# Kernel tuning notes

Measured on AMD Instinct MI355X. Metric: run time of the kernel, lower is better.

Reference implementation:

```python
import jax, jax.numpy as jnp
import numpy as np

B, R, C, D = 8, 64, 16, 128  # batch, num_rows(taxa), patch_num, embed_dim


def _linear_init(key, fan_in, fan_out):
    lim = 1.0 / np.sqrt(fan_in)
    kw, kb = jax.random.split(key)
    W = jax.random.uniform(kw, (fan_in, fan_out), jnp.float32, -lim, lim)
    b = jax.random.uniform(kb, (fan_out,), jnp.float32, -lim, lim)
    return W, b


def setup_inputs() -> dict:
    key = jax.random.key(0)
    ks = jax.random.split(key, 8)
    row_np, col_np = np.triu_indices(R, k=1)  # n = R*(R-1)/2 = 2016 pairs
    hW, hb = _linear_init(ks[1], D, D)
    gW, gb = _linear_init(ks[2], D, D)
    qW, qb = _linear_init(ks[3], D, D)
    kW, kb = _linear_init(ks[4], D, D)
    s1W, s1b = _linear_init(ks[5], D, D)
    s2W, s2b = _linear_init(ks[6], D, 1)
    return {
        "batch_input": jax.random.normal(ks[0], (B, R, C, D), jnp.float32),
        "seq_mask": jnp.ones((B, 1, C), jnp.float32),
        "row": jnp.asarray(row_np, jnp.int32),
        "col": jnp.asarray(col_np, jnp.int32),
        "hW": hW, "hb": hb, "gW": gW, "gb": gb,
        "qW": qW, "qb": qb, "kW": kW, "kb": kb,
        "s1W": s1W, "s1b": s1b, "s2W": s2W, "s2b": s2b,
    }


def reference(batch_input, seq_mask, row, col,
              hW, hb, gW, gb, qW, qb, kW, kb, s1W, s1b, s2W, s2b):
    b, r, c, d = batch_input.shape
    n = row.shape[0]
    # pairwise gather: x_i, x_j -> [b, n, c, d]
    x_i = batch_input[:, row]
    x_j = batch_input[:, col]
    # sigmoid gate fusion of the pair
    h = (x_i - x_j) @ hW + hb
    z = jax.nn.sigmoid(h)
    x = z * x_i + (1.0 - z) * x_j
    # masked global attention over the batch_input 'memory' (r > 2 branch)
    q = x @ qW + qb                    # [b, n, c, d]
    k = batch_input @ kW + kb          # [b, r, c, d]
    scale = 1.0 / np.sqrt(d * c).astype(np.float32)
    alpha = jnp.einsum('bncd,brcd->bnr', q, k) * scale
    # -inf at (pair n, rows row[n] and col[n]); equivalent to += -inf on finite scores
    neg_mask = (jnp.zeros((n, r), bool)
                .at[jnp.arange(n), row].set(True)
                .at[jnp.arange(n), col].set(True))
    alpha = jnp.where(neg_mask[None], -jnp.inf, alpha)
    alpha = jax.nn.softmax(alpha, axis=-1)
    x_glob = jnp.einsum('bnr,brcd->bncd', alpha, batch_input)
    g = x_glob @ gW + gb
    w = jax.nn.sigmoid(g)
    x = (1.0 - w) * x + w * x_glob
    # s_out: Linear -> GELU(exact) -> Linear(d,1), then mask and reduce over c
    s = jax.nn.gelu(x @ s1W + s1b, approximate=False) @ s2W + s2b  # [b, n, c, 1]
    scores = s[..., 0] * seq_mask       # seq_mask [b,1,c] broadcasts over n
    return scores.sum(-1)               # [b, n]
```

## Files before the change

kernel.cpp:

```cpp
#include <hip/hip_runtime.h>
#include <hip/hip_bf16.h>
#include <math.h>

#define B_    8
#define R_    64
#define C_    16
#define D_    128
#define NPAIR 2016
#define CD    2048
#define PG    32
#define NPG   63
#define XSTR  136
#define LSTR  68
#define NEG_BIG (-1e30f)
#define SCALE 0.022097086912079608f

typedef __attribute__((ext_vector_type(8))) short short8;
typedef __attribute__((ext_vector_type(4))) float float4v;

#define WMH  0u
#define WML  16384u
#define WSH  98304u
#define VECO 131072u
#define QBKO 131592u
#define MO   132616u
#define XTO  1181192u
#define GTO  2229768u
#define HO   3278344u

__device__ __forceinline__ unsigned short f2b(float f){
    union { float f; unsigned int u; } v; v.f = f;
    const unsigned int r = v.u + 0x7FFFu + ((v.u >> 16) & 1u);
    return (unsigned short)(r >> 16);
}
__device__ __forceinline__ float b2f(unsigned short u){
    union { unsigned int i; float f; } v; v.i = ((unsigned int)u) << 16; return v.f;
}
__device__ __forceinline__ float lo2f(unsigned int u){
    union { unsigned int i; float f; } v; v.i = u << 16; return v.f;
}
__device__ __forceinline__ float hif2f(unsigned int u){
    union { unsigned int i; float f; } v; v.i = u & 0xffff0000u; return v.f;
}
__device__ __forceinline__ unsigned int pack2(float a, float b){
    unsigned int r;
    asm("v_cvt_pk_bf16_f32 %0, %1, %2" : "=v"(r) : "v"(a), "v"(b));
    return r;
}
__device__ __forceinline__ unsigned short f2b1(float a){
    unsigned int r;
    asm("v_cvt_pk_bf16_f32 %0, %1, %1" : "=v"(r) : "v"(a));
    return (unsigned short)r;
}
__device__ __forceinline__ void split_bf(float v, float* hi, float* lo){
    union { float f; unsigned int u; } x; x.f = v;
    const unsigned int r = (x.u + 0x7FFFu + ((x.u >> 16) & 1u)) & 0xffff0000u;
    union { unsigned int u; float f; } h; h.u = r;
    *hi = h.f; *lo = v - h.f;
}
__device__ __forceinline__ void splitw(float v, short* h, short* l){
    union { float f; unsigned int u; } x; x.f = v;
    const unsigned int rh = (x.u + 0x7FFFu + ((x.u >> 16) & 1u)) & 0xffff0000u;
    union { unsigned int u; float f; } hf; hf.u = rh;
    *h = (short)(rh >> 16);
    *l = (short)f2b(v - hf.f);
}
__device__ __forceinline__ float sigmoid_safe(float x){
    return __builtin_amdgcn_rcpf(1.f + __expf(-x));
}
__device__ __forceinline__ float gelu_tanh(float x){
    const float u = x*x;
    const float g2 = x*(1.5957691216057308f + 0.07135481627159f*u);
    return x * sigmoid_safe(g2);
}

__global__ __launch_bounds__(256) void k_prepA(
    const float* __restrict__ qW, const float* __restrict__ qb,
    const float* __restrict__ kW, const float* __restrict__ kb,
    unsigned short* __restrict__ ws)
{
    const int bid = blockIdx.x, t = threadIdx.x;
    if (bid < 64){
        __shared__ float sKW[2][128];
        const int e0 = bid*2;
        sKW[t>>7][t&127] = kW[(e0 + (t>>7))*128 + (t&127)];
        __syncthreads();
        const int e = t>>7, d = t&127;
        const float* qr = qW + d*128;
        const float* kr = sKW[e];
        float acc = 0.f;
        #pragma unroll 8
        for (int g = 0; g < 128; g += 4){
            const float4 qv = *reinterpret_cast<const float4*>(qr + g);
            acc += qv.x*kr[g] + qv.y*kr[g+1] + qv.z*kr[g+2] + qv.w*kr[g+3];
        }
        float hi, lo; split_bf(acc, &hi, &lo);
        ws[WMH + d*128 + (e0+e)] = f2b(hi);
        ws[WML + d*128 + (e0+e)] = f2b(lo);
    } else {
        float* vec = (float*)(ws + VECO);
        if (t < 128){
            float a1 = 0.f, a2 = 0.f;
            #pragma unroll 8
            for (int g = 0; g < 128; g += 4){
                const float4 q4 = *reinterpret_cast<const float4*>(qW + t*128 + g);
                const float4 k4 = *reinterpret_cast<const float4*>(kW + t*128 + g);
                const float4 kb4 = *reinterpret_cast<const float4*>(kb + g);
                const float4 qb4 = *reinterpret_cast<const float4*>(qb + g);
                a1 += q4.x*kb4.x + q4.y*kb4.y + q4.z*kb4.z + q4.w*kb4.w;
                a2 += k4.x*qb4.x + k4.y*qb4.y + k4.z*qb4.z + k4.w*qb4.w;
            }
            vec[t] = a1;
            vec[128 + t] = a2;
        } else if (t == 128){
            float a = 0.f;
            for (int g = 0; g < 128; ++g) a = fmaf(qb[g], kb[g], a);
            vec[256] = a;
        }
    }
}

__global__ __launch_bounds__(512) void k_prepB(const float* __restrict__ x,
        const float* __restrict__ hW, const float* __restrict__ gW,
        const float* __restrict__ gb, const float* __restrict__ s1W,
        unsigned short* __restrict__ ws)
{
    __shared__ __align__(16) unsigned short smem[8832];
    __shared__ float sQ[4];
    const int bid = blockIdx.x, t = threadIdx.x;
    const int w = t >> 6, lane = t & 63, l15 = lane & 15, quad = lane >> 4;

    if (bid < 128){
        unsigned short* sH = smem;
        const int br0 = bid * 4;
        const float* kqf = (const float*)(ws + VECO) + 128;
        const float* mbf = (const float*)(ws + VECO);
        if (t < 4) sQ[t] = 0.f;
        __syncthreads();
        float qacc[4] = {0.f, 0.f, 0.f, 0.f};
        #pragma unroll
        for (int i = 0; i < 4; ++i){
            const int flat = (t + 512*i)*4;
            const int lr = i;
            const int cd = flat & 2047;
            const float4 v = *reinterpret_cast<const float4*>(x + (size_t)(br0+lr)*CD + cd);
            const int ad = (lr*16 + (cd>>7))*XSTR + lr*8 + (cd & 127);
            uint2 uh;
            uh.x = pack2(v.x, v.y); uh.y = pack2(v.z, v.w);
            *reinterpret_cast<uint2*>(sH + ad) = uh;
            const float4 kq4 = *reinterpret_cast<const float4*>(kqf + (cd & 127));
            qacc[i] = v.x*kq4.x + v.y*kq4.y + v.z*kq4.z + v.w*kq4.w;
        }
        #pragma unroll
        for (int i = 0; i < 4; ++i){
            float s = qacc[i];
            #pragma unroll
            for (int off = 1; off < 64; off <<= 1) s += __shfl_xor(s, off);
            if (lane == 0) atomicAdd(&sQ[i], s);
        }
        __syncthreads();
        {
            const float bv = mbf[w*16 + l15];
            float4v acc[4];
            #pragma unroll
            for (int mt = 0; mt < 4; ++mt){ float4v d = {bv,bv,bv,bv}; acc[mt] = d; }
            #pragma unroll
            for (int ks = 0; ks < 4; ++ks){
                const int ko = ks*32 + quad*8;
                const int bd = (w*16 + l15)*128 + ko;
                const short8 bh = *reinterpret_cast<const short8*>(ws + WMH + bd);
                const short8 bl = *reinterpret_cast<const short8*>(ws + WML + bd);
                #pragma unroll
                for (int mt = 0; mt < 4; ++mt){
                    const int ad = (mt*16 + l15)*XSTR + mt*8 + ko;
                    const short8 ah = *reinterpret_cast<const short8*>(sH + ad);
                    float4v d = acc[mt];
                    d = __builtin_amdgcn_mfma_f32_16x16x32_bf16(ah, bh, d, 0,0,0);
                    d = __builtin_amdgcn_mfma_f32_16x16x32_bf16(ah, bl, d, 0,0,0);
                    acc[mt] = d;
                }
            }
            const int f = w*16 + l15;
            #pragma unroll
            for (int mt = 0; mt < 4; ++mt)
            #pragma unroll
            for (int e = 0; e < 4; ++e){
                const int c = quad*4 + e;
                ws[MO + (size_t)(br0+mt)*CD + c*128 + f] = f2b(acc[mt][e]);
            }
            if (t < 4){
                const float s0 = ((const float*)(ws + VECO))[256];
                ((float*)(ws + QBKO))[br0 + t] = sQ[t] + 16.f*s0;
            }
        }
        {
            const int n = w*16 + l15;
            float4v acc[4];
            #pragma unroll
            for (int mt = 0; mt < 4; ++mt){ float4v z = {0.f,0.f,0.f,0.f}; acc[mt] = z; }
            #pragma unroll
            for (int ks = 0; ks < 4; ++ks){
                const int ko = ks*32 + quad*8;
                short8 bh, bl;
                #pragma unroll
                for (int j = 0; j < 8; ++j){
                    short hh, ll;
                    splitw(hW[(size_t)(ko+j)*128 + n], &hh, &ll);
                    bh[j] = hh; bl[j] = ll;
                }
                #pragma unroll
                for (int mt = 0; mt < 4; ++mt){
                    const int ad = (mt*16 + l15)*XSTR + mt*8 + ko;
                    const short8 ah = *reinterpret_cast<const short8*>(sH + ad);
                    float4v d = acc[mt];
                    d = __builtin_amdgcn_mfma_f32_16x16x32_bf16(ah, bh, d, 0,0,0);
                    d = __builtin_amdgcn_mfma_f32_16x16x32_bf16(ah, bl, d, 0,0,0);
                    acc[mt] = d;
                }
            }
            #pragma unroll
            for (int mt = 0; mt < 4; ++mt)
            #pragma unroll
            for (int e = 0; e < 4; ++e){
                const int c = quad*4 + e;
                ws[HO + (size_t)(br0+mt)*CD + c*128 + n] = f2b(acc[mt][e]);
            }
        }
    } else if (bid < 256){
        unsigned short* tileB = smem;
        const int gidx = bid - 128;
        const int b = gidx >> 4, cd0 = (gidx & 15)*128;
        #pragma unroll
        for (int i = 0; i < 16; ++i){
            const int idx = i*512 + t;
            const int r = idx >> 7, dd = idx & 127;
            tileB[r*138 + dd] = f2b(x[(size_t)(b*64 + r)*CD + cd0 + dd]);
        }
        __syncthreads();
        {
            const unsigned int base = XTO + (unsigned int)(b*2048 + cd0)*64;
            #pragma unroll
            for (int j = 0; j < 16; ++j){
                const int idx = j*512 + t;
                const int cc = idx >> 6, r = idx & 63;
                ws[base + cc*64 + r] = tileB[r*138 + cc];
            }
        }
        const int fA = w*16 + l15;
        float4v acc[4];
        #pragma unroll
        for (int nt = 0; nt < 4; ++nt){ float4v z = {0.f,0.f,0.f,0.f}; acc[nt] = z; }
        #pragma unroll
        for (int ks = 0; ks < 4; ++ks){
            const int ko = ks*32 + quad*8;
            short8 ah, al;
            #pragma unroll
            for (int j = 0; j < 8; ++j){
                short hh, ll;
                splitw(gW[(size_t)(ko+j)*128 + fA], &hh, &ll);
                ah[j] = hh; al[j] = ll;
            }
            #pragma unroll
            for (int nt = 0; nt < 4; ++nt){
                const short8 bb = *reinterpret_cast<const short8*>(tileB + (nt*16 + l15)*138 + ko);
                float4v d = acc[nt];
                d = __builtin_amdgcn_mfma_f32_16x16x32_bf16(ah, bb, d, 0,0,0);
                d = __builtin_amdgcn_mfma_f32_16x16x32_bf16(al, bb, d, 0,0,0);
                acc[nt] = d;
            }
        }
        #pragma unroll
        for (int nt = 0; nt < 4; ++nt)
        #pragma unroll
        for (int e = 0; e < 4; ++e){
            const int f = w*16 + quad*4 + e;
            const float val = acc[nt][e] + gb[f];
            ws[GTO + (size_t)(b*2048 + cd0 + f)*64 + nt*16 + l15] = f2b(val);
        }
    } else {
        const int gid = (bid - 256)*4096 + t;
        #pragma unroll
        for (int i = 0; i < 8; ++i){
            const int g = gid + i*512;
            const int n = g >> 7, k = g & 127;
            ws[WSH + g] = f2b(s1W[k*128 + n]);
        }
    }
}

__global__ __launch_bounds__(1024, 4) void k_main(
    const float* __restrict__ x, const float* __restrict__ seq_mask,
    const int* __restrict__ row, const int* __restrict__ col,
    const float* __restrict__ hb, const float* __restrict__ s1b,
    const float* __restrict__ s2W, const float* __restrict__ s2b,
    const unsigned short* __restrict__ ws, float* __restrict__ out)
{
    __shared__ __align__(16) unsigned short sX[512*XSTR + 256];
    __shared__ __align__(16) unsigned short sAl[32*72];
    __shared__ float sLog[32*LSTR];
    __shared__ float sOut[PG];
    __shared__ float sMask[16];
    __shared__ int srp[PG], scp[PG];

    const int t = threadIdx.x;
    const int w = t >> 6, lane = t & 63, l15 = lane & 15, quad = lane >> 4;
    const int b = blockIdx.x, p0 = blockIdx.y * PG;
    const float* xb = x + (size_t)b * R_ * CD;
    const unsigned short* Hb = ws + HO + (size_t)b * R_ * CD;

    if (t < PG){ srp[t] = row[p0+t]; scp[t] = col[p0+t]; sOut[t] = 0.f; }
    if (t >= 32 && t < 48) sMask[t-32] = seq_mask[b*C_ + (t-32)];
    for (int i = t; i < 32*72; i += 1024) sAl[i] = 0;
    for (int i = t; i < 32*LSTR; i += 1024) sLog[i] = 0.f;
    __syncthreads();

    #pragma unroll 4
    for (int i = 0; i < 16; ++i){
        const int flat = (t + 1024*i)*4;
        const int p = flat >> 11, cd = flat & 2047;
        const int ri = srp[p], ci = scp[p];
        const float4 xi = *reinterpret_cast<const float4*>(xb + (size_t)ri*CD + cd);
        const float4 xj = *reinterpret_cast<const float4*>(xb + (size_t)ci*CD + cd);
        const uint2 Hi2 = *reinterpret_cast<const uint2*>(Hb + (size_t)ri*CD + cd);
        const uint2 Hj2 = *reinterpret_cast<const uint2*>(Hb + (size_t)ci*CD + cd);
        const float4 h4 = *reinterpret_cast<const float4*>(hb + (cd & 127));
        const float z0 = sigmoid_safe(lo2f(Hi2.x)  - lo2f(Hj2.x)  + h4.x);
        const float z1 = sigmoid_safe(hif2f(Hi2.x) - hif2f(Hj2.x) + h4.y);
        const float z2 = sigmoid_safe(lo2f(Hi2.y)  - lo2f(Hj2.y)  + h4.z);
        const float z3 = sigmoid_safe(hif2f(Hi2.y) - hif2f(Hj2.y) + h4.w);
        const float v0 = xj.x + z0*(xi.x - xj.x);
        const float v1 = xj.y + z1*(xi.y - xj.y);
        const float v2 = xj.z + z2*(xi.z - xj.z);
        const float v3 = xj.w + z3*(xi.w - xj.w);
        const int ad = (p*16 + (cd>>7))*XSTR + p*8 + (cd & 127);
        uint2 uv; uv.x = pack2(v0,v1); uv.y = pack2(v2,v3);
        *reinterpret_cast<uint2*>(sX + ad) = uv;
    }
    __syncthreads();

    {
        const int rt = w & 3, kh = w >> 2;
        const int r = rt*16 + l15;
        const unsigned short* Mr = ws + MO + ((size_t)b*64 + r)*CD + kh*512;
        float4v d0a = {0.f,0.f,0.f,0.f}, d0b = {0.f,0.f,0.f,0.f};
        float4v d1a = {0.f,0.f,0.f,0.f}, d1b = {0.f,0.f,0.f,0.f};
        #pragma unroll
        for (int h = 0; h < 2; ++h){
            short8 bhr[8];
            #pragma unroll
            for (int u = 0; u < 8; ++u)
                bhr[u] = *reinterpret_cast<const short8*>(Mr + (h*8+u)*32 + quad*8);
            #pragma unroll
            for (int u = 0; u < 8; ++u){
                const int k = kh*512 + (h*8+u)*32 + quad*8;
                const int khi = k >> 7, klo = k & 127;
                const int pA = l15, pB = 16 + l15;
                const short8 ahA = *reinterpret_cast<const short8*>(
                    sX + (pA*16 + khi)*XSTR + pA*8 + klo);
                const short8 ahB = *reinterpret_cast<const short8*>(
                    sX + (pB*16 + khi)*XSTR + pB*8 + klo);
                if (u & 1){
                    d0b = __builtin_amdgcn_mfma_f32_16x16x32_bf16(ahA, bhr[u], d0b, 0,0,0);
                    d1b = __builtin_amdgcn_mfma_f32_16x16x32_bf16(ahB, bhr[u], d1b, 0,0,0);
                } else {
                    d0a = __builtin_amdgcn_mfma_f32_16x16x32_bf16(ahA, bhr[u], d0a, 0,0,0);
                    d1a = __builtin_amdgcn_mfma_f32_16x16x32_bf16(ahB, bhr[u], d1a, 0,0,0);
                }
            }
        }
        const float4v dA = d0a + d0b;
        const float4v dB = d1a + d1b;
        #pragma unroll
        for (int e = 0; e < 4; ++e){
            const int pp = quad*4 + e;
            atomicAdd(&sLog[pp*LSTR + r], dA[e]);
            atomicAdd(&sLog[(16+pp)*LSTR + r], dB[e]);
        }
    }
    __syncthreads();

    const unsigned short* XTb = ws + XTO + (size_t)b * CD * 64;
    const unsigned short* GTb = ws + GTO + (size_t)b * CD * 64;
    short8 px0[2], px1[2], pg0[2], pg1[2];
    #pragma unroll
    for (int j = 0; j < 2; ++j){
        const int cd = w*128 + j*16 + l15;
        px0[j] = *reinterpret_cast<const short8*>(XTb + (size_t)cd*64 + quad*8);
        px1[j] = *reinterpret_cast<const short8*>(XTb + (size_t)cd*64 + 32 + quad*8);
        pg0[j] = *reinterpret_cast<const short8*>(GTb + (size_t)cd*64 + quad*8);
        pg1[j] = *reinterpret_cast<const short8*>(GTb + (size_t)cd*64 + 32 + quad*8);
    }

    if (t < 512){
        const int pp = t >> 4, l = t & 15;
        const int ri = srp[pp], ci = scp[pp];
        const float* qbk = (const float*)(ws + QBKO);
        float v[4]; float m = NEG_BIG;
        #pragma unroll
        for (int k = 0; k < 4; ++k){
            const int r = l + 16*k;
            float lv = (sLog[pp*LSTR + r] + qbk[b*64 + r]) * SCALE;
            if (r == ri || r == ci) lv = NEG_BIG;
            v[k] = lv; m = fmaxf(m, lv);
        }
        #pragma unroll
        for (int s = 1; s < 16; s <<= 1) m = fmaxf(m, __shfl_xor(m, s));
        float e4[4]; float sum = 0.f;
        #pragma unroll
        for (int k = 0; k < 4; ++k){
            const int r = l + 16*k;
            const bool masked = (r == ri || r == ci);
            const float e = masked ? 0.f : __expf(fmaxf(v[k]-m, -80.f));
            e4[k] = e; sum += e;
        }
        #pragma unroll
        for (int s = 1; s < 16; s <<= 1) sum += __shfl_xor(sum, s);
        const float inv = __builtin_amdgcn_rcpf(sum);
        #pragma unroll
        for (int k = 0; k < 4; ++k) sAl[pp*72 + l + 16*k] = f2b1(e4[k]*inv);
    }
    __syncthreads();

    {
        const short8 AhA0 = *reinterpret_cast<const short8*>(sAl + l15*72 + quad*8);
        const short8 AhA1 = *reinterpret_cast<const short8*>(sAl + l15*72 + 32 + quad*8);
        const short8 AhB0 = *reinterpret_cast<const short8*>(sAl + (16+l15)*72 + quad*8);
        const short8 AhB1 = *reinterpret_cast<const short8*>(sAl + (16+l15)*72 + 32 + quad*8);
        #pragma unroll
        for (int j = 0; j < 8; ++j){
            const int s = j & 1;
            float4v dxA = {0.f,0.f,0.f,0.f}, dgA = {0.f,0.f,0.f,0.f};
            float4v dxB = {0.f,0.f,0.f,0.f}, dgB = {0.f,0.f,0.f,0.f};
            dxA = __builtin_amdgcn_mfma_f32_16x16x32_bf16(AhA0, px0[s], dxA, 0,0,0);
            dxA = __builtin_amdgcn_mfma_f32_16x16x32_bf16(AhA1, px1[s], dxA, 0,0,0);
            dgA = __builtin_amdgcn_mfma_f32_16x16x32_bf16(AhA0, pg0[s], dgA, 0,0,0);
            dgA = __builtin_amdgcn_mfma_f32_16x16x32_bf16(AhA1, pg1[s], dgA, 0,0,0);
            dxB = __builtin_amdgcn_mfma_f32_16x16x32_bf16(AhB0, px0[s], dxB, 0,0,0);
            dxB = __builtin_amdgcn_mfma_f32_16x16x32_bf16(AhB1, px1[s], dxB, 0,0,0);
            dgB = __builtin_amdgcn_mfma_f32_16x16x32_bf16(AhB0, pg0[s], dgB, 0,0,0);
            dgB = __builtin_amdgcn_mfma_f32_16x16x32_bf16(AhB1, pg1[s], dgB, 0,0,0);
            if (j + 2 < 8){
                const int cd2 = w*128 + (j+2)*16 + l15;
                px0[s] = *reinterpret_cast<const short8*>(XTb + (size_t)cd2*64 + quad*8);
                px1[s] = *reinterpret_cast<const short8*>(XTb + (size_t)cd2*64 + 32 + quad*8);
                pg0[s] = *reinterpret_cast<const short8*>(GTb + (size_t)cd2*64 + quad*8);
                pg1[s] = *reinterpret_cast<const short8*>(GTb + (size_t)cd2*64 + 32 + quad*8);
            }
            const int cd = w*128 + j*16 + l15;
            const int khi = cd >> 7, klo = cd & 127;
            #pragma unroll
            for (int e = 0; e < 4; ++e){
                const int ppA = quad*4 + e;
                const int adA = (ppA*16 + khi)*XSTR + ppA*8 + klo;
                const float wvA = sigmoid_safe(dgA[e]);
                const float xoA = b2f(sX[adA]);
                sX[adA] = f2b1((1.f - wvA)*xoA + wvA*dxA[e]);
                const int ppB = 16 + quad*4 + e;
                const int adB = (ppB*16 + khi)*XSTR + ppB*8 + klo;
                const float wvB = sigmoid_safe(dgB[e]);
                const float xoB = b2f(sX[adB]);
                sX[adB] = f2b1((1.f - wvB)*xoB + wvB*dxB[e]);
            }
        }
    }
    __syncthreads();

    {
        const int mh = w >> 3, nw = w & 7;
        float4v acc16[16];
        const float bv = s1b[nw*16 + l15];
        #pragma unroll
        for (int mt = 0; mt < 16; ++mt){ float4v d = {bv,bv,bv,bv}; acc16[mt] = d; }
        short8 bh4[4];
        #pragma unroll
        for (int ks = 0; ks < 4; ++ks)
            bh4[ks] = *reinterpret_cast<const short8*>(ws + WSH + (nw*16 + l15)*128 + ks*32 + quad*8);
        #pragma unroll
        for (int ks = 0; ks < 4; ++ks){
            const int ko = ks*32 + quad*8;
            #pragma unroll
            for (int mt = 0; mt < 16; ++mt){
                const int p = mh*16 + mt;
                const short8 a = *reinterpret_cast<const short8*>(sX + (p*16 + l15)*XSTR + p*8 + ko);
                acc16[mt] = __builtin_amdgcn_mfma_f32_16x16x32_bf16(a, bh4[ks], acc16[mt], 0,0,0);
            }
        }
        const float s2v = s2W[nw*16 + l15];
        const float mk0 = sMask[quad*4+0], mk1 = sMask[quad*4+1];
        const float mk2 = sMask[quad*4+2], mk3 = sMask[quad*4+3];
        float psum[16];
        #pragma unroll
        for (int mt = 0; mt < 16; ++mt){
            float s = gelu_tanh(acc16[mt][0]) * mk0;
            s += gelu_tanh(acc16[mt][1]) * mk1;
            s += gelu_tanh(acc16[mt][2]) * mk2;
            s += gelu_tanh(acc16[mt][3]) * mk3;
            psum[mt] = s * s2v;
        }
        #pragma unroll
        for (int s = 1; s < 64; s <<= 1)
            #pragma unroll
            for (int mt = 0; mt < 16; ++mt) psum[mt] += __shfl_xor(psum[mt], s);
        if (lane == 0){
            #pragma unroll
            for (int mt = 0; mt < 16; ++mt) atomicAdd(&sOut[mh*16 + mt], psum[mt]);
        }
    }
    __syncthreads();

    if (t < PG){
        float msum = 0.f;
        #pragma unroll
        for (int c = 0; c < 16; ++c) msum += sMask[c];
        out[(size_t)b*NPAIR + p0 + t] = sOut[t] + s2b[0]*msum;
    }
}

extern "C" void kernel_launch(void* const* d_in, const int* in_sizes, int n_in,
                              void* d_out, int out_size, void* d_ws, size_t ws_size,
                              hipStream_t stream)
{
    const float* x    = (const float*)d_in[0];
    const float* mask = (const float*)d_in[1];
    const int*   row  = (const int*)d_in[2];
    const int*   col  = (const int*)d_in[3];
    const float* hW  = (const float*)d_in[4];  const float* hb  = (const float*)d_in[5];
    const float* gW  = (const float*)d_in[6];  const float* gb  = (const float*)d_in[7];
    const float* qW  = (const float*)d_in[8];  const float* qb  = (const float*)d_in[9];
    const float* kW  = (const float*)d_in[10]; const float* kb  = (const float*)d_in[11];
    const float* s1W = (const float*)d_in[12]; const float* s1b = (const float*)d_in[13];
    const float* s2W = (const float*)d_in[14]; const float* s2b = (const float*)d_in[15];

    unsigned short* ws = (unsigned short*)d_ws;

    k_prepA<<<65, 256, 0, stream>>>(qW, qb, kW, kb, ws);
    k_prepB<<<260, 512, 0, stream>>>(x, hW, gW, gb, s1W, ws);
    k_main<<<dim3(B_, NPG), 1024, 0, stream>>>(x, mask, row, col,
                                               hb, s1b, s2W, s2b,
                                               ws, (float*)d_out);
}
```

Baseline: 204.1 us.

## Prefetch global MFMA operands early and widen the pair-gate gather to 8 elements

Global loads of the key-projection operands (first half), the XT/GT operands and the s1W fragments are issued earlier, before barriers or in the middle of preceding compute, so their latency overlaps the gather and MFMA work. The gate-fusion gather now handles 8 elements per thread with wider loads and 16-byte LDS stores. The redundant zeroing of sAl is removed. This raises register pressure from the extra live short8 fragments, which may reduce occupancy or cause spills in a 1024-thread block.

```diff
diff --git a/kernel.cpp b/kernel.cpp
--- a/kernel.cpp
+++ b/kernel.cpp
@@ -308,88 +308,119 @@
     const float* xb = x + (size_t)b * R_ * CD;
     const unsigned short* Hb = ws + HO + (size_t)b * R_ * CD;
 
+    const int rt = w & 3, kh = w >> 2;
+    const int r2 = rt*16 + l15;
+    const unsigned short* Mr = ws + MO + ((size_t)b*64 + r2)*CD + kh*512;
+    short8 bhr0[8];
+    #pragma unroll
+    for (int u = 0; u < 8; ++u)
+        bhr0[u] = *reinterpret_cast<const short8*>(Mr + u*32 + quad*8);
+
     if (t < PG){ srp[t] = row[p0+t]; scp[t] = col[p0+t]; sOut[t] = 0.f; }
     if (t >= 32 && t < 48) sMask[t-32] = seq_mask[b*C_ + (t-32)];
-    for (int i = t; i < 32*72; i += 1024) sAl[i] = 0;
     for (int i = t; i < 32*LSTR; i += 1024) sLog[i] = 0.f;
     __syncthreads();
 
-    #pragma unroll 4
-    for (int i = 0; i < 16; ++i){
-        const int flat = (t + 1024*i)*4;
+    #pragma unroll
+    for (int i = 0; i < 8; ++i){
+        const int flat = (t + 1024*i)*8;
         const int p = flat >> 11, cd = flat & 2047;
         const int ri = srp[p], ci = scp[p];
-        const float4 xi = *reinterpret_cast<const float4*>(xb + (size_t)ri*CD + cd);
-        const float4 xj = *reinterpret_cast<const float4*>(xb + (size_t)ci*CD + cd);
-        const uint2 Hi2 = *reinterpret_cast<const uint2*>(Hb + (size_t)ri*CD + cd);
-        const uint2 Hj2 = *reinterpret_cast<const uint2*>(Hb + (size_t)ci*CD + cd);
-        const float4 h4 = *reinterpret_cast<const float4*>(hb + (cd & 127));
-        const float z0 = sigmoid_safe(lo2f(Hi2.x)  - lo2f(Hj2.x)  + h4.x);
-        const float z1 = sigmoid_safe(hif2f(Hi2.x) - hif2f(Hj2.x) + h4.y);
-        const float z2 = sigmoid_safe(lo2f(Hi2.y)  - lo2f(Hj2.y)  + h4.z);
-        const float z3 = sigmoid_safe(hif2f(Hi2.y) - hif2f(Hj2.y) + h4.w);
-        const float v0 = xj.x + z0*(xi.x - xj.x);
-        const float v1 = xj.y + z1*(xi.y - xj.y);
-        const float v2 = xj.z + z2*(xi.z - xj.z);
-        const float v3 = xj.w + z3*(xi.w - xj.w);
+        const float* xip = xb + (size_t)ri*CD + cd;
+        const float* xjp = xb + (size_t)ci*CD + cd;
+        const float4 xi0 = *reinterpret_cast<const float4*>(xip);
+        const float4 xi1 = *reinterpret_cast<const float4*>(xip + 4);
+        const float4 xj0 = *reinterpret_cast<const float4*>(xjp);
+        const float4 xj1 = *reinterpret_cast<const float4*>(xjp + 4);
+        const uint4 Hi4 = *reinterpret_cast<const uint4*>(Hb + (size_t)ri*CD + cd);
+        const uint4 Hj4 = *reinterpret_cast<const uint4*>(Hb + (size_t)ci*CD + cd);
+        const float4 h40 = *reinterpret_cast<const float4*>(hb + (cd & 127));
+        const float4 h41 = *reinterpret_cast<const float4*>(hb + (cd & 127) + 4);
+        const float z0 = sigmoid_safe(lo2f(Hi4.x)  - lo2f(Hj4.x)  + h40.x);
+        const float z1 = sigmoid_safe(hif2f(Hi4.x) - hif2f(Hj4.x) + h40.y);
+        const float z2 = sigmoid_safe(lo2f(Hi4.y)  - lo2f(Hj4.y)  + h40.z);
+        const float z3 = sigmoid_safe(hif2f(Hi4.y) - hif2f(Hj4.y) + h40.w);
+        const float z4 = sigmoid_safe(lo2f(Hi4.z)  - lo2f(Hj4.z)  + h41.x);
+        const float z5 = sigmoid_safe(hif2f(Hi4.z) - hif2f(Hj4.z) + h41.y);
+        const float z6 = sigmoid_safe(lo2f(Hi4.w)  - lo2f(Hj4.w)  + h41.z);
+        const float z7 = sigmoid_safe(hif2f(Hi4.w) - hif2f(Hj4.w) + h41.w);
+        const float v0 = xj0.x + z0*(xi0.x - xj0.x);
+        const float v1 = xj0.y + z1*(xi0.y - xj0.y);
+        const float v2 = xj0.z + z2*(xi0.z - xj0.z);
+        const float v3 = xj0.w + z3*(xi0.w - xj0.w);
+        const float v4 = xj1.x + z4*(xi1.x - xj1.x);
+        const float v5 = xj1.y + z5*(xi1.y - xj1.y);
+        const float v6 = xj1.z + z6*(xi1.z - xj1.z);
+        const float v7 = xj1.w + z7*(xi1.w - xj1.w);
         const int ad = (p*16 + (cd>>7))*XSTR + p*8 + (cd & 127);
-        uint2 uv; uv.x = pack2(v0,v1); uv.y = pack2(v2,v3);
-        *reinterpret_cast<uint2*>(sX + ad) = uv;
-    }
-    __syncthreads();
-
-    {
-        const int rt = w & 3, kh = w >> 2;
-        const int r = rt*16 + l15;
-        const unsigned short* Mr = ws + MO + ((size_t)b*64 + r)*CD + kh*512;
-        float4v d0a = {0.f,0.f,0.f,0.f}, d0b = {0.f,0.f,0.f,0.f};
-        float4v d1a = {0.f,0.f,0.f,0.f}, d1b = {0.f,0.f,0.f,0.f};
-        #pragma unroll
-        for (int h = 0; h < 2; ++h){
-            short8 bhr[8];
-            #pragma unroll
-            for (int u = 0; u < 8; ++u)
-                bhr[u] = *reinterpret_cast<const short8*>(Mr + (h*8+u)*32 + quad*8);
-            #pragma unroll
-            for (int u = 0; u < 8; ++u){
-                const int k = kh*512 + (h*8+u)*32 + quad*8;
-                const int khi = k >> 7, klo = k & 127;
-                const int pA = l15, pB = 16 + l15;
-                const short8 ahA = *reinterpret_cast<const short8*>(
-                    sX + (pA*16 + khi)*XSTR + pA*8 + klo);
-                const short8 ahB = *reinterpret_cast<const short8*>(
-                    sX + (pB*16 + khi)*XSTR + pB*8 + klo);
-                if (u & 1){
-                    d0b = __builtin_amdgcn_mfma_f32_16x16x32_bf16(ahA, bhr[u], d0b, 0,0,0);
-                    d1b = __builtin_amdgcn_mfma_f32_16x16x32_bf16(ahB, bhr[u], d1b, 0,0,0);
-                } else {
-                    d0a = __builtin_amdgcn_mfma_f32_16x16x32_bf16(ahA, bhr[u], d0a, 0,0,0);
-                    d1a = __builtin_amdgcn_mfma_f32_16x16x32_bf16(ahB, bhr[u], d1a, 0,0,0);
-                }
-            }
-        }
-        const float4v dA = d0a + d0b;
-        const float4v dB = d1a + d1b;
-        #pragma unroll
-        for (int e = 0; e < 4; ++e){
-            const int pp = quad*4 + e;
-            atomicAdd(&sLog[pp*LSTR + r], dA[e]);
-            atomicAdd(&sLog[(16+pp)*LSTR + r], dB[e]);
-        }
+        uint4 uv;
+        uv.x = pack2(v0,v1); uv.y = pack2(v2,v3);
+        uv.z = pack2(v4,v5); uv.w = pack2(v6,v7);
+        *reinterpret_cast<uint4*>(sX + ad) = uv;
     }
     __syncthreads();
 
     const unsigned short* XTb = ws + XTO + (size_t)b * CD * 64;
     const unsigned short* GTb = ws + GTO + (size_t)b * CD * 64;
     short8 px0[2], px1[2], pg0[2], pg1[2];
-    #pragma unroll
-    for (int j = 0; j < 2; ++j){
-        const int cd = w*128 + j*16 + l15;
-        px0[j] = *reinterpret_cast<const short8*>(XTb + (size_t)cd*64 + quad*8);
-        px1[j] = *reinterpret_cast<const short8*>(XTb + (size_t)cd*64 + 32 + quad*8);
-        pg0[j] = *reinterpret_cast<const short8*>(GTb + (size_t)cd*64 + quad*8);
-        pg1[j] = *reinterpret_cast<const short8*>(GTb + (size_t)cd*64 + 32 + quad*8);
-    }
+
+    {
+        short8 bhr1[8];
+        #pragma unroll
+        for (int u = 0; u < 8; ++u)
+            bhr1[u] = *reinterpret_cast<const short8*>(Mr + (8+u)*32 + quad*8);
+        float4v d0a = {0.f,0.f,0.f,0.f}, d0b = {0.f,0.f,0.f,0.f};
+        float4v d1a = {0.f,0.f,0.f,0.f}, d1b = {0.f,0.f,0.f,0.f};
+        #pragma unroll
+        for (int u = 0; u < 8; ++u){
+            const int k = kh*512 + u*32 + quad*8;
+            const int khi = k >> 7, klo = k & 127;
+            const short8 ahA = *reinterpret_cast<const short8*>(
+                sX + (l15*16 + khi)*XSTR + l15*8 + klo);
+            const short8 ahB = *reinterpret_cast<const short8*>(
+                sX + ((16+l15)*16 + khi)*XSTR + (16+l15)*8 + klo);
+            if (u & 1){
+                d0b = __builtin_amdgcn_mfma_f32_16x16x32_bf16(ahA, bhr0[u], d0b, 0,0,0);
+                d1b = __builtin_amdgcn_mfma_f32_16x16x32_bf16(ahB, bhr0[u], d1b, 0,0,0);
+            } else {
+                d0a = __builtin_amdgcn_mfma_f32_16x16x32_bf16(ahA, bhr0[u], d0a, 0,0,0);
+                d1a = __builtin_amdgcn_mfma_f32_16x16x32_bf16(ahB, bhr0[u], d1a, 0,0,0);
+            }
+        }
+        #pragma unroll
+        for (int j = 0; j < 2; ++j){
+            const int cd = w*128 + j*16 + l15;
+            px0[j] = *reinterpret_cast<const short8*>(XTb + (size_t)cd*64 + quad*8);
+            px1[j] = *reinterpret_cast<const short8*>(XTb + (size_t)cd*64 + 32 + quad*8);
+            pg0[j] = *reinterpret_cast<const short8*>(GTb + (size_t)cd*64 + quad*8);
+            pg1[j] = *reinterpret_cast<const short8*>(GTb + (size_t)cd*64 + 32 + quad*8);
+        }
+        #pragma unroll
+        for (int u = 0; u < 8; ++u){
+            const int k = kh*512 + (8+u)*32 + quad*8;
+            const int khi = k >> 7, klo = k & 127;
+            const short8 ahA = *reinterpret_cast<const short8*>(
+                sX + (l15*16 + khi)*XSTR + l15*8 + klo);
+            const short8 ahB = *reinterpret_cast<const short8*>(
+                sX + ((16+l15)*16 + khi)*XSTR + (16+l15)*8 + klo);
+            if (u & 1){
+                d0b = __builtin_amdgcn_mfma_f32_16x16x32_bf16(ahA, bhr1[u], d0b, 0,0,0);
+                d1b = __builtin_amdgcn_mfma_f32_16x16x32_bf16(ahB, bhr1[u], d1b, 0,0,0);
+            } else {
+                d0a = __builtin_amdgcn_mfma_f32_16x16x32_bf16(ahA, bhr1[u], d0a, 0,0,0);
+                d1a = __builtin_amdgcn_mfma_f32_16x16x32_bf16(ahB, bhr1[u], d1a, 0,0,0);
+            }
+        }
+        const float4v dA = d0a + d0b;
+        const float4v dB = d1a + d1b;
+        #pragma unroll
+        for (int e = 0; e < 4; ++e){
+            const int pp = quad*4 + e;
+            atomicAdd(&sLog[pp*LSTR + r2], dA[e]);
+            atomicAdd(&sLog[(16+pp)*LSTR + r2], dB[e]);
+        }
+    }
+    __syncthreads();
 
     if (t < 512){
         const int pp = t >> 4, l = t & 15;
@@ -420,6 +451,12 @@
         for (int k = 0; k < 4; ++k) sAl[pp*72 + l + 16*k] = f2b1(e4[k]*inv);
     }
     __syncthreads();
+
+    const int mh = w >> 3, nw = w & 7;
+    short8 bh4[4];
+    #pragma unroll
+    for (int ks = 0; ks < 4; ++ks)
+        bh4[ks] = *reinterpret_cast<const short8*>(ws + WSH + (nw*16 + l15)*128 + ks*32 + quad*8);
 
     {
         const short8 AhA0 = *reinterpret_cast<const short8*>(sAl + l15*72 + quad*8);
@@ -466,15 +503,10 @@
     __syncthreads();
 
     {
-        const int mh = w >> 3, nw = w & 7;
         float4v acc16[16];
         const float bv = s1b[nw*16 + l15];
         #pragma unroll
         for (int mt = 0; mt < 16; ++mt){ float4v d = {bv,bv,bv,bv}; acc16[mt] = d; }
-        short8 bh4[4];
-        #pragma unroll
-        for (int ks = 0; ks < 4; ++ks)
-            bh4[ks] = *reinterpret_cast<const short8*>(ws + WSH + (nw*16 + l15)*128 + ks*32 + quad*8);
         #pragma unroll
         for (int ks = 0; ks < 4; ++ks){
             const int ko = ks*32 + quad*8;
```

New measurement: 196.7 us. 1.04x faster.
